# Kernel tuning notes

Hardware: AMD Instinct MI355X
Metric: run time of the kernel (lower is better)

Reference implementation:

```python
import jax, jax.numpy as jnp
import numpy as np

B, C, H, W = 4, 128, 128, 128
HEADS, DHEAD = 8, C // 8
N = H * W
NEG_SLOPE = 0.2
LN_EPS = 1e-5


def _build_grid_edges(h, w):
    # 3x3 neighborhood including self (matches the torch double loop),
    # then append N extra self loops (add_self_loops in the module).
    rows, cols = [], []
    for r in range(h):
        for c in range(w):
            idx = r * w + c
            for dr in (-1, 0, 1):
                for dc in (-1, 0, 1):
                    nr, nc = r + dr, c + dc
                    if 0 <= nr < h and 0 <= nc < w:
                        rows.append(idx)
                        cols.append(nr * w + nc)
    rows += list(range(h * w))
    cols += list(range(h * w))
    return np.asarray(rows, np.int32), np.asarray(cols, np.int32)

_SRC_NP, _DST_NP = _build_grid_edges(H, W)  # PyG: messages flow src -> dst
SRC = jnp.asarray(_SRC_NP)
DST = jnp.asarray(_DST_NP)


def setup_inputs() -> dict:
    key = jax.random.key(0)
    ks = jax.random.split(key, 7)
    s_lin = 1.0 / np.sqrt(C)
    return {
        "x": jax.random.normal(ks[0], (B, C, H, W), jnp.float32),
        "W_lin": jax.random.normal(ks[1], (C, HEADS * DHEAD), jnp.float32) * s_lin,
        "att_src": jax.random.normal(ks[2], (HEADS, DHEAD), jnp.float32) * s_lin,
        "att_dst": jax.random.normal(ks[3], (HEADS, DHEAD), jnp.float32) * s_lin,
        "bias": jnp.zeros((C,), jnp.float32),
        "gamma": jnp.ones((C,), jnp.float32),
        "beta": jnp.zeros((C,), jnp.float32),
    }


def _gat_forward(x, W_lin, att_src, att_dst, bias, gamma, beta):
    b = x.shape[0]
    x_nodes = x.reshape(b, C, N).transpose(0, 2, 1)            # [B,N,C]
    xp = (x_nodes @ W_lin).reshape(b, N, HEADS, DHEAD)          # [B,N,H,D]
    a_src = jnp.einsum('bnhd,hd->bnh', xp, att_src)             # [B,N,H]
    a_dst = jnp.einsum('bnhd,hd->bnh', xp, att_dst)
    score = jax.nn.leaky_relu(a_src[:, SRC] + a_dst[:, DST], NEG_SLOPE)  # [B,E,H]

    def seg_softmax(s):  # [E,H] softmax over edges grouped by DST
        m = jax.ops.segment_max(s, DST, num_segments=N)
        e = jnp.exp(s - m[DST])
        den = jax.ops.segment_sum(e, DST, num_segments=N)
        return e / den[DST]

    alpha = jax.vmap(seg_softmax)(score)                        # [B,E,H]
    msg = xp[:, SRC] * alpha[..., None]                         # [B,E,H,D]
    agg = jax.vmap(lambda m: jax.ops.segment_sum(m, DST, num_segments=N))(msg)
    out = agg.reshape(b, N, C) + bias                           # GATConv bias
    out = jax.nn.elu(out)
    # LayerNorm over channel dim
    mu = out.mean(-1, keepdims=True)
    var = out.var(-1, keepdims=True)
    out = (out - mu) * jax.lax.rsqrt(var + LN_EPS) * gamma + beta
    return out.transpose(0, 2, 1).reshape(b, C, H, W)


def reference(x, W_lin, att_src, att_dst, bias, gamma, beta):
    return _gat_forward(x, W_lin, att_src, att_dst, bias, gamma, beta)
```

## Files before the change

### kernel.cpp

```cpp
#include <hip/hip_runtime.h>
#include <stdint.h>

#define BATCH  4
#define CCH    128
#define GRID_H 128
#define GRID_W 128
#define NNODE  (GRID_H*GRID_W)
#define NHEAD  8
#define DH     16
#define WPAD   68
#define WROWS  144

typedef __attribute__((ext_vector_type(8))) short short8;
typedef __attribute__((ext_vector_type(4))) float f32x4;
typedef __attribute__((ext_vector_type(4))) unsigned u32x4;

__device__ inline unsigned short f2bf(float f){
    unsigned u = __float_as_uint(f);
    return (unsigned short)((u + 0x7FFFu + ((u >> 16) & 1u)) >> 16);
}
__device__ inline unsigned packbf(float a, float b){
    return (unsigned)f2bf(a) | ((unsigned)f2bf(b) << 16);
}
__device__ inline float bflo(unsigned u){ return __uint_as_float(u << 16); }
__device__ inline float bfhi(unsigned u){ return __uint_as_float(u & 0xFFFF0000u); }

__global__ void kW(const float* __restrict__ Wl, const float* __restrict__ attS,
                   const float* __restrict__ attD, unsigned* __restrict__ Wb)
{
    __shared__ float Wa[8][16];
    const int t = threadIdx.x;
    const int cbase = blockIdx.x * 8;
    if (t < 128){
        int cl = t >> 4, j = t & 15;
        const float* av = (j < 8 ? attS + j*DH : attD + (j-8)*DH);
        const float* wr = Wl + (size_t)(cbase + cl)*CCH + (j & 7)*DH;
        float s = 0.f;
        #pragma unroll
        for (int d = 0; d < DH; ++d) s += wr[d]*av[d];
        Wa[cl][j] = s;
    }
    __syncthreads();
    for (int it = 0; it < 3; ++it){
        int flat = it*256 + t;
        if (flat < 576){
            int k2l = flat / 144, co = flat % 144;
            int k2 = blockIdx.x*4 + k2l;
            float w0, w1;
            if (co < CCH){
                w0 = Wl[(size_t)(2*k2)*CCH + co];
                w1 = Wl[(size_t)(2*k2+1)*CCH + co];
            } else {
                w0 = Wa[2*k2l][co-CCH];
                w1 = Wa[2*k2l+1][co-CCH];
            }
            Wb[co*WPAD + k2] = packbf(w0, w1);
        }
    }
}

__global__ __launch_bounds__(256, 2) void kA(
    const float* __restrict__ x, const unsigned* __restrict__ Wbg,
    unsigned short* __restrict__ xpb, float* __restrict__ scb)
{
    __shared__ __align__(16) unsigned WbL[WROWS*WPAD];
    __shared__ __align__(16) unsigned Xa[128*WPAD];

    const int t  = threadIdx.x;
    const int b  = blockIdx.y;
    const int n0 = blockIdx.x * 128;

    #pragma unroll
    for (int it = 0; it < 10; ++it){
        int f4 = it*256 + t;
        if (f4 < (WROWS*WPAD)/4)
            *(u32x4*)(&WbL[f4*4]) = *(const u32x4*)(Wbg + (size_t)f4*4);
    }
    const float* xb = x + (size_t)b*CCH*NNODE + n0;
    {
        const int g = t & 31, c2b = t >> 5;
        #pragma unroll
        for (int it = 0; it < 8; ++it){
            int c2 = c2b + it*8;
            const float* p0 = xb + (size_t)(2*c2)*NNODE + 4*g;
            f32x4 v0 = *(const f32x4*)p0;
            f32x4 v1 = *(const f32x4*)(p0 + NNODE);
            #pragma unroll
            for (int i = 0; i < 4; ++i)
                Xa[(4*g+i)*WPAD + c2] = packbf(v0[i], v1[i]);
        }
    }
    __syncthreads();

    const int w = t >> 6, lane = t & 63;
    const int col = lane & 15, q = lane >> 4;

    f32x4 acc[2][9];
    #pragma unroll
    for (int mi = 0; mi < 2; ++mi)
        #pragma unroll
        for (int ct = 0; ct < 9; ++ct) acc[mi][ct] = (f32x4)(0.f);

    union U { u32x4 u; short8 s; };
    #pragma unroll
    for (int kc = 0; kc < 4; ++kc){
        const int kof = kc*16 + q*4;
        U fa0, fa1;
        fa0.u = *(const u32x4*)(&Xa[((2*w+0)*16+col)*WPAD + kof]);
        fa1.u = *(const u32x4*)(&Xa[((2*w+1)*16+col)*WPAD + kof]);
        #pragma unroll
        for (int ct = 0; ct < 9; ++ct){
            U fb; fb.u = *(const u32x4*)(&WbL[(ct*16+col)*WPAD + kof]);
            acc[0][ct] = __builtin_amdgcn_mfma_f32_16x16x32_bf16(fa0.s, fb.s, acc[0][ct], 0, 0, 0);
            acc[1][ct] = __builtin_amdgcn_mfma_f32_16x16x32_bf16(fa1.s, fb.s, acc[1][ct], 0, 0, 0);
        }
    }

    unsigned short* xr = xpb + (size_t)b*NNODE*CCH;
    float*          sr = scb + (size_t)b*NNODE*16;
    const int sidx = (col < 8) ? 2*col : 2*(col-8)+1;
    #pragma unroll
    for (int mi = 0; mi < 2; ++mi){
        #pragma unroll
        for (int r = 0; r < 4; ++r){
            const int n = n0 + (2*w+mi)*16 + q*4 + r;
            #pragma unroll
            for (int ct = 0; ct < 8; ++ct)
                xr[(size_t)n*CCH + ct*16 + col] = f2bf(acc[mi][ct][r]);
            sr[(size_t)n*16 + sidx] = acc[mi][8][r];
        }
    }
}

__global__ __launch_bounds__(256, 4) void kB(
    const unsigned short* __restrict__ xpb, const float* __restrict__ scb,
    const float* __restrict__ bias, const float* __restrict__ gamma,
    const float* __restrict__ beta, float* __restrict__ out)
{
    __shared__ float outT[CCH][65];
    const int t = threadIdx.x, w = t >> 6, lane = t & 63;
    const int h2 = lane >> 5, l2 = lane & 31;
    const int b  = blockIdx.y;
    const int n0 = blockIdx.x * 64;
    const uint2*  xvb = (const uint2*)(xpb + (size_t)b*NNODE*CCH);
    const float2* scB = (const float2*)(scb + (size_t)b*NNODE*16);
    const int h = l2 >> 2;
    const f32x4 bi = *(const f32x4*)(bias  + 4*l2);
    const f32x4 ga = *(const f32x4*)(gamma + 4*l2);
    const f32x4 be = *(const f32x4*)(beta  + 4*l2);

    for (int i = 0; i < 8; ++i){
        const int nl = w*16 + 2*i + h2;
        const int n  = n0 + nl;
        const int rr = n >> 7, cc = n & 127;
        const bool vU = rr > 0, vD = rr < GRID_H-1, vL = cc > 0, vR = cc < GRID_W-1;

        bool val[9]; int src[9];
        #pragma unroll
        for (int e = 0; e < 9; ++e){
            const int dr = e/3 - 1, dc = e%3 - 1;
            const bool vr_ = (dr < 0) ? vU : (dr > 0 ? vD : true);
            const bool vc_ = (dc < 0) ? vL : (dc > 0 ? vR : true);
            val[e] = vr_ && vc_;
            src[e] = val[e] ? (n + dr*GRID_W + dc) : n;
        }
        float2 sc[9];
        #pragma unroll
        for (int e = 0; e < 9; ++e) sc[e] = scB[src[e]*8 + h];
        uint2 xv[9];
        #pragma unroll
        for (int e = 0; e < 9; ++e) xv[e] = xvb[(size_t)src[e]*32 + l2];

        const float ad = sc[4].y;
        float s[9], m = -1e30f;
        #pragma unroll
        for (int e = 0; e < 9; ++e){
            float sv = sc[e].x + ad;
            sv = fmaxf(sv, 0.2f*sv);
            s[e] = val[e] ? sv : -1e30f;
            m = fmaxf(m, s[e]);
        }
        float wt[9], den = 0.f;
        #pragma unroll
        for (int e = 0; e < 9; ++e){
            float ex = __expf(s[e] - m);
            ex = val[e] ? ex : 0.f;
            wt[e] = ex; den += ex;
        }
        den += wt[4];
        const float inv = __builtin_amdgcn_rcpf(den);

        float a0 = 0.f, a1 = 0.f, a2 = 0.f, a3 = 0.f;
        #pragma unroll
        for (int e = 0; e < 9; ++e){
            float f = wt[e] * inv;
            if (e == 4) f += f;
            a0 += f * bflo(xv[e].x);
            a1 += f * bfhi(xv[e].x);
            a2 += f * bflo(xv[e].y);
            a3 += f * bfhi(xv[e].y);
        }

        float o0 = a0 + bi[0], o1 = a1 + bi[1], o2 = a2 + bi[2], o3 = a3 + bi[3];
        o0 = o0 > 0.f ? o0 : __expf(o0) - 1.f;
        o1 = o1 > 0.f ? o1 : __expf(o1) - 1.f;
        o2 = o2 > 0.f ? o2 : __expf(o2) - 1.f;
        o3 = o3 > 0.f ? o3 : __expf(o3) - 1.f;

        float sm = (o0 + o1) + (o2 + o3);
        float sq = o0*o0 + o1*o1 + o2*o2 + o3*o3;
        #pragma unroll
        for (int off = 1; off <= 16; off <<= 1){
            sm += __shfl_xor(sm, off, 64);
            sq += __shfl_xor(sq, off, 64);
        }
        const float mu  = sm * (1.f/128.f);
        float var = sq * (1.f/128.f) - mu*mu;
        var = var < 0.f ? 0.f : var;
        const float rstd = __builtin_amdgcn_rsqf(var + 1e-5f);
        outT[4*l2+0][nl] = (o0 - mu)*rstd*ga[0] + be[0];
        outT[4*l2+1][nl] = (o1 - mu)*rstd*ga[1] + be[1];
        outT[4*l2+2][nl] = (o2 - mu)*rstd*ga[2] + be[2];
        outT[4*l2+3][nl] = (o3 - mu)*rstd*ga[3] + be[3];
    }
    __syncthreads();

    float* ob = out + (size_t)b*CCH*NNODE + n0;
    #pragma unroll
    for (int it = 0; it < 32; ++it){
        int c = it*4 + w;
        ob[(size_t)c*NNODE + lane] = outT[c][lane];
    }
}

extern "C" void kernel_launch(void* const* d_in, const int* in_sizes, int n_in,
                              void* d_out, int out_size, void* d_ws, size_t ws_size,
                              hipStream_t stream)
{
    const float* x    = (const float*)d_in[0];
    const float* Wl   = (const float*)d_in[1];
    const float* attS = (const float*)d_in[2];
    const float* attD = (const float*)d_in[3];
    const float* bias = (const float*)d_in[4];
    const float* gamma= (const float*)d_in[5];
    const float* beta = (const float*)d_in[6];
    float* out = (float*)d_out;

    unsigned short* xpb = (unsigned short*)d_ws;
    float*          scb = (float*)(xpb + (size_t)BATCH*NNODE*CCH);
    unsigned*       Wb  = (unsigned*)(scb + (size_t)BATCH*NNODE*16);

    kW<<<dim3(16), 256, 0, stream>>>(Wl, attS, attD, Wb);
    kA<<<dim3(NNODE/128, BATCH), 256, 0, stream>>>(x, Wb, xpb, scb);
    kB<<<dim3(NNODE/64, BATCH), 256, 0, stream>>>(xpb, scb, bias, gamma, beta, out);
}
```

Before: 122.4 us.

## Load x directly into MFMA fragments and double-buffer neighbor gathers

In kA, the shared-memory staging of the input tile is removed. Each lane now loads its x values straight from global memory into registers, packs them to bf16 MFMA fragments, and prefetches the next k-chunk while the current one computes. This frees LDS and raises the occupancy hint to 3. In kB, the per-node neighbor gathers are software-pipelined: loads for node i+1 are issued before node i is computed, which hides gather latency at the cost of extra registers (occupancy hint drops from 4 to 3). The direct x loads are strided per lane and less coalesced than the old vectorized staging, so memory efficiency may suffer.

New measurement: 118.0 us. 1.04x faster.

```diff
diff --git a/kernel.cpp b/kernel.cpp
--- a/kernel.cpp
+++ b/kernel.cpp
@@ -59,12 +59,11 @@
     }
 }
 
-__global__ __launch_bounds__(256, 2) void kA(
+__global__ __launch_bounds__(256, 3) void kA(
     const float* __restrict__ x, const unsigned* __restrict__ Wbg,
     unsigned short* __restrict__ xpb, float* __restrict__ scb)
 {
     __shared__ __align__(16) unsigned WbL[WROWS*WPAD];
-    __shared__ __align__(16) unsigned Xa[128*WPAD];
 
     const int t  = threadIdx.x;
     const int b  = blockIdx.y;
@@ -76,24 +75,13 @@
         if (f4 < (WROWS*WPAD)/4)
             *(u32x4*)(&WbL[f4*4]) = *(const u32x4*)(Wbg + (size_t)f4*4);
     }
-    const float* xb = x + (size_t)b*CCH*NNODE + n0;
-    {
-        const int g = t & 31, c2b = t >> 5;
-        #pragma unroll
-        for (int it = 0; it < 8; ++it){
-            int c2 = c2b + it*8;
-            const float* p0 = xb + (size_t)(2*c2)*NNODE + 4*g;
-            f32x4 v0 = *(const f32x4*)p0;
-            f32x4 v1 = *(const f32x4*)(p0 + NNODE);
-            #pragma unroll
-            for (int i = 0; i < 4; ++i)
-                Xa[(4*g+i)*WPAD + c2] = packbf(v0[i], v1[i]);
-        }
-    }
     __syncthreads();
 
     const int w = t >> 6, lane = t & 63;
     const int col = lane & 15, q = lane >> 4;
+    const float* xb = x + (size_t)b*CCH*NNODE;
+    const int nA = n0 + (2*w+0)*16 + col;
+    const int nB = n0 + (2*w+1)*16 + col;
 
     f32x4 acc[2][9];
     #pragma unroll
@@ -101,19 +89,40 @@
         #pragma unroll
         for (int ct = 0; ct < 9; ++ct) acc[mi][ct] = (f32x4)(0.f);
 
+    float xrA[8], xrB[8], x2A[8], x2B[8];
+    #pragma unroll
+    for (int j = 0; j < 8; ++j){
+        const size_t co = (size_t)(q*8 + j)*NNODE;
+        xrA[j] = xb[co + nA];
+        xrB[j] = xb[co + nB];
+    }
+
     union U { u32x4 u; short8 s; };
     #pragma unroll
     for (int kc = 0; kc < 4; ++kc){
+        if (kc < 3){
+            #pragma unroll
+            for (int j = 0; j < 8; ++j){
+                const size_t co = (size_t)((kc+1)*32 + q*8 + j)*NNODE;
+                x2A[j] = xb[co + nA];
+                x2B[j] = xb[co + nB];
+            }
+        }
+        U fa0, fa1;
+        #pragma unroll
+        for (int i = 0; i < 4; ++i){
+            fa0.u[i] = packbf(xrA[2*i], xrA[2*i+1]);
+            fa1.u[i] = packbf(xrB[2*i], xrB[2*i+1]);
+        }
         const int kof = kc*16 + q*4;
-        U fa0, fa1;
-        fa0.u = *(const u32x4*)(&Xa[((2*w+0)*16+col)*WPAD + kof]);
-        fa1.u = *(const u32x4*)(&Xa[((2*w+1)*16+col)*WPAD + kof]);
         #pragma unroll
         for (int ct = 0; ct < 9; ++ct){
             U fb; fb.u = *(const u32x4*)(&WbL[(ct*16+col)*WPAD + kof]);
             acc[0][ct] = __builtin_amdgcn_mfma_f32_16x16x32_bf16(fa0.s, fb.s, acc[0][ct], 0, 0, 0);
             acc[1][ct] = __builtin_amdgcn_mfma_f32_16x16x32_bf16(fa1.s, fb.s, acc[1][ct], 0, 0, 0);
         }
+        #pragma unroll
+        for (int j = 0; j < 8; ++j){ xrA[j] = x2A[j]; xrB[j] = x2B[j]; }
     }
 
     unsigned short* xr = xpb + (size_t)b*NNODE*CCH;
@@ -132,7 +141,28 @@
     }
 }
 
-__global__ __launch_bounds__(256, 4) void kB(
+__device__ inline void kb_issue(int n, const float2* __restrict__ scB,
+                                const uint2* __restrict__ xvb, int h, int l2,
+                                int* vm, float2 sc[9], uint2 xv[9])
+{
+    const int rr = n >> 7, cc = n & 127;
+    const bool vU = rr > 0, vD = rr < GRID_H-1, vL = cc > 0, vR = cc < GRID_W-1;
+    int m = 0;
+    #pragma unroll
+    for (int e = 0; e < 9; ++e){
+        const int dr = e/3 - 1, dc = e%3 - 1;
+        const bool vr_ = (dr < 0) ? vU : (dr > 0 ? vD : true);
+        const bool vc_ = (dc < 0) ? vL : (dc > 0 ? vR : true);
+        const bool v = vr_ && vc_;
+        const int src = v ? (n + dr*GRID_W + dc) : n;
+        m |= ((int)v) << e;
+        sc[e] = scB[src*8 + h];
+        xv[e] = xvb[(size_t)src*32 + l2];
+    }
+    *vm = m;
+}
+
+__global__ __launch_bounds__(256, 3) void kB(
     const unsigned short* __restrict__ xpb, const float* __restrict__ scb,
     const float* __restrict__ bias, const float* __restrict__ gamma,
     const float* __restrict__ beta, float* __restrict__ out)
@@ -149,80 +179,79 @@
     const f32x4 ga = *(const f32x4*)(gamma + 4*l2);
     const f32x4 be = *(const f32x4*)(beta  + 4*l2);
 
-    for (int i = 0; i < 8; ++i){
-        const int nl = w*16 + 2*i + h2;
-        const int n  = n0 + nl;
-        const int rr = n >> 7, cc = n & 127;
-        const bool vU = rr > 0, vD = rr < GRID_H-1, vL = cc > 0, vR = cc < GRID_W-1;
-
-        bool val[9]; int src[9];
-        #pragma unroll
-        for (int e = 0; e < 9; ++e){
-            const int dr = e/3 - 1, dc = e%3 - 1;
-            const bool vr_ = (dr < 0) ? vU : (dr > 0 ? vD : true);
-            const bool vc_ = (dc < 0) ? vL : (dc > 0 ? vR : true);
-            val[e] = vr_ && vc_;
-            src[e] = val[e] ? (n + dr*GRID_W + dc) : n;
-        }
-        float2 sc[9];
-        #pragma unroll
-        for (int e = 0; e < 9; ++e) sc[e] = scB[src[e]*8 + h];
-        uint2 xv[9];
-        #pragma unroll
-        for (int e = 0; e < 9; ++e) xv[e] = xvb[(size_t)src[e]*32 + l2];
-
-        const float ad = sc[4].y;
-        float s[9], m = -1e30f;
-        #pragma unroll
-        for (int e = 0; e < 9; ++e){
-            float sv = sc[e].x + ad;
-            sv = fmaxf(sv, 0.2f*sv);
-            s[e] = val[e] ? sv : -1e30f;
-            m = fmaxf(m, s[e]);
-        }
-        float wt[9], den = 0.f;
-        #pragma unroll
-        for (int e = 0; e < 9; ++e){
-            float ex = __expf(s[e] - m);
-            ex = val[e] ? ex : 0.f;
-            wt[e] = ex; den += ex;
-        }
-        den += wt[4];
-        const float inv = __builtin_amdgcn_rcpf(den);
-
-        float a0 = 0.f, a1 = 0.f, a2 = 0.f, a3 = 0.f;
-        #pragma unroll
-        for (int e = 0; e < 9; ++e){
-            float f = wt[e] * inv;
-            if (e == 4) f += f;
-            a0 += f * bflo(xv[e].x);
-            a1 += f * bfhi(xv[e].x);
-            a2 += f * bflo(xv[e].y);
-            a3 += f * bfhi(xv[e].y);
-        }
-
-        float o0 = a0 + bi[0], o1 = a1 + bi[1], o2 = a2 + bi[2], o3 = a3 + bi[3];
-        o0 = o0 > 0.f ? o0 : __expf(o0) - 1.f;
-        o1 = o1 > 0.f ? o1 : __expf(o1) - 1.f;
-        o2 = o2 > 0.f ? o2 : __expf(o2) - 1.f;
-        o3 = o3 > 0.f ? o3 : __expf(o3) - 1.f;
-
-        float sm = (o0 + o1) + (o2 + o3);
-        float sq = o0*o0 + o1*o1 + o2*o2 + o3*o3;
-        #pragma unroll
-        for (int off = 1; off <= 16; off <<= 1){
-            sm += __shfl_xor(sm, off, 64);
-            sq += __shfl_xor(sq, off, 64);
-        }
-        const float mu  = sm * (1.f/128.f);
-        float var = sq * (1.f/128.f) - mu*mu;
-        var = var < 0.f ? 0.f : var;
-        const float rstd = __builtin_amdgcn_rsqf(var + 1e-5f);
-        outT[4*l2+0][nl] = (o0 - mu)*rstd*ga[0] + be[0];
-        outT[4*l2+1][nl] = (o1 - mu)*rstd*ga[1] + be[1];
-        outT[4*l2+2][nl] = (o2 - mu)*rstd*ga[2] + be[2];
-        outT[4*l2+3][nl] = (o3 - mu)*rstd*ga[3] + be[3];
-    }
+    float2 scP[2][9]; uint2 xvP[2][9]; int vmP[2];
+
+    #define NODE(i) (n0 + w*16 + 2*(i) + h2)
+    kb_issue(NODE(0), scB, xvb, h, l2, &vmP[0], scP[0], xvP[0]);
+
+    #pragma unroll
+    for (int ii = 0; ii < 4; ++ii){
+        #pragma unroll
+        for (int ph = 0; ph < 2; ++ph){
+            const int i = 2*ii + ph;
+            const int cur = i & 1;
+            if (i + 1 < 8)
+                kb_issue(NODE(i+1), scB, xvb, h, l2, &vmP[cur^1], scP[cur^1], xvP[cur^1]);
+
+            const int vm = vmP[cur];
+            const float2* sc = scP[cur];
+            const uint2*  xv = xvP[cur];
+            const int nl = w*16 + 2*i + h2;
+
+            const float ad = sc[4].y;
+            float s[9], mx = -1e30f;
+            #pragma unroll
+            for (int e = 0; e < 9; ++e){
+                float sv = sc[e].x + ad;
+                sv = fmaxf(sv, 0.2f*sv);
+                s[e] = ((vm >> e) & 1) ? sv : -1e30f;
+                mx = fmaxf(mx, s[e]);
+            }
+            float wt[9], den = 0.f;
+            #pragma unroll
+            for (int e = 0; e < 9; ++e){
+                float ex = __expf(s[e] - mx);
+                ex = ((vm >> e) & 1) ? ex : 0.f;
+                wt[e] = ex; den += ex;
+            }
+            den += wt[4];
+            const float inv = __builtin_amdgcn_rcpf(den);
+
+            float a0 = 0.f, a1 = 0.f, a2 = 0.f, a3 = 0.f;
+            #pragma unroll
+            for (int e = 0; e < 9; ++e){
+                float f = wt[e] * inv;
+                if (e == 4) f += f;
+                a0 += f * bflo(xv[e].x);
+                a1 += f * bfhi(xv[e].x);
+                a2 += f * bflo(xv[e].y);
+                a3 += f * bfhi(xv[e].y);
+            }
+
+            float o0 = a0 + bi[0], o1 = a1 + bi[1], o2 = a2 + bi[2], o3 = a3 + bi[3];
+            o0 = o0 > 0.f ? o0 : __expf(o0) - 1.f;
+            o1 = o1 > 0.f ? o1 : __expf(o1) - 1.f;
+            o2 = o2 > 0.f ? o2 : __expf(o2) - 1.f;
+            o3 = o3 > 0.f ? o3 : __expf(o3) - 1.f;
+
+            float sm = (o0 + o1) + (o2 + o3);
+            float sq = o0*o0 + o1*o1 + o2*o2 + o3*o3;
+            #pragma unroll
+            for (int off = 1; off <= 16; off <<= 1){
+                sm += __shfl_xor(sm, off, 64);
+                sq += __shfl_xor(sq, off, 64);
+            }
+            const float mu  = sm * (1.f/128.f);
+            float var = sq * (1.f/128.f) - mu*mu;
+            var = var < 0.f ? 0.f : var;
+            const float rstd = __builtin_amdgcn_rsqf(var + 1e-5f);
+            outT[4*l2+0][nl] = (o0 - mu)*rstd*ga[0] + be[0];
+            outT[4*l2+1][nl] = (o1 - mu)*rstd*ga[1] + be[1];
+            outT[4*l2+2][nl] = (o2 - mu)*rstd*ga[2] + be[2];
+            outT[4*l2+3][nl] = (o3 - mu)*rstd*ga[3] + be[3];
+        }
+    }
+    #undef NODE
     __syncthreads();
 
     float* ob = out + (size_t)b*CCH*NNODE + n0;
```
